# Kernel tuning notes

Hardware: AMD Instinct MI355X
Metric: run time of the kernel (lower is better)

Reference implementation:

```python
import jax, jax.numpy as jnp
import numpy as np

E = 8        # num experts
TOPK = 2
H = 1024     # hidden size
F = 4096     # ffn hidden size
SL, BS = 2048, 2
TOKENS = SL * BS
N = TOKENS * TOPK          # flattened routing assignments
CAP = (TOPK * TOKENS) // E # expert_capacity with capacity_factor=1.0


def setup_inputs() -> dict:
    key = jax.random.key(0)
    ks = jax.random.split(key, 6)
    x = jax.random.normal(ks[0], (SL, BS, H), jnp.float32)
    scores = jax.random.uniform(ks[1], (TOKENS, E), dtype=jnp.float32)
    expert_weights = jax.random.uniform(ks[2], (TOKENS, TOPK), dtype=jnp.float32)
    top_experts = jax.random.randint(ks[3], (TOKENS, TOPK), 0, E, dtype=jnp.int32)
    w1 = jax.random.normal(ks[4], (E, H, F), jnp.float32) * 0.02
    w2 = jax.random.normal(ks[5], (E, F, H), jnp.float32) * 0.02
    bias = jnp.zeros((H,), jnp.float32)
    return {"x": x, "scores": scores, "expert_weights": expert_weights,
            "top_experts": top_experts, "w1": w1, "w2": w2, "bias": bias}


def reference(x, scores, expert_weights, top_experts, w1, w2, bias):
    # --- indices_and_bins: stable sort tokens by expert, histogram, cumsum ---
    te = top_experts.reshape(-1)          # [N] int
    ew = expert_weights.reshape(-1)       # [N]
    xf = x.reshape(-1, H)                 # [TOKENS, H]

    indices = jnp.argsort(te)             # stable sort -> permutation [N]
    bin_ids = te[indices]                 # sorted expert ids [N]
    tpe = jax.ops.segment_sum(jnp.ones_like(te), te, num_segments=E)  # tokens per expert
    bins = jnp.cumsum(tpe)                # inclusive cumsum
    starts = bins - tpe                   # start offset of each expert's bin
    pos = jnp.arange(N) - starts[bin_ids] # position within expert bin [N]
    valid = pos < CAP                     # capacity drop mask
    tok = indices // TOPK                 # source token row for each assignment

    # --- binned_gather: [E, CAP, H], zero padded, tokens beyond capacity dropped ---
    dst = jnp.where(valid, pos, CAP)      # out-of-range -> dropped via mode='drop'
    buf = jnp.zeros((E, CAP, H), x.dtype).at[bin_ids, dst].set(xf[tok], mode='drop')

    # --- grouped MLP: per-expert gelu FFN ---
    h = jax.nn.gelu(jnp.einsum('ech,ehf->ecf', buf, w1), approximate=False)
    y = jnp.einsum('ecf,efh->ech', h, w2)

    # --- binned_scatter: weighted un-permute back to token order ---
    vals = y[bin_ids, jnp.where(valid, pos, 0)]                      # [N, H]
    w = jnp.where(valid, ew[indices], 0.0)[:, None]
    out = jnp.zeros((TOKENS, H), x.dtype).at[tok].add(vals * w)

    return out.reshape(x.shape) + bias
```

## Files before the change

### kernel.cpp

```cpp
#include <hip/hip_runtime.h>
#include <hip/hip_bf16.h>
#include <math.h>

#define NE 8
#define TOPK 2
#define HD 1024
#define FD 4096
#define NTOK 4096
#define NASSIGN 8192
#define CAP 1024

typedef __attribute__((ext_vector_type(8))) short short8;
typedef __attribute__((ext_vector_type(4))) float f32x4;
typedef __attribute__((ext_vector_type(4))) unsigned short us4;
typedef __attribute__((ext_vector_type(4))) unsigned int u32x4;

__device__ __forceinline__ unsigned short f2bf(float f) {
  unsigned u = __float_as_uint(f);
  u += 0x7fffu + ((u >> 16) & 1u);
  return (unsigned short)(u >> 16);
}

__device__ __forceinline__ void load_lds16(const void* g, void* l) {
  __builtin_amdgcn_global_load_lds((const __attribute__((address_space(1))) void*)g,
                                   (__attribute__((address_space(3))) void*)l, 16, 0, 0);
}

__device__ __forceinline__ unsigned swz(unsigned b) {
  return b ^ (((b >> 7) & 3u) << 4);
}

__global__ __launch_bounds__(256)
void transpose_convert(const float* __restrict__ W, unsigned short* __restrict__ Wt,
                       int R, int C) {
  __shared__ float tile[64][65];
  int e = blockIdx.z;
  W  += (size_t)e * R * C;
  Wt += (size_t)e * R * C;
  int c0 = blockIdx.x * 64, r0 = blockIdx.y * 64;
  int tx = threadIdx.x & 15, ty = threadIdx.x >> 4;
#pragma unroll
  for (int i = 0; i < 4; ++i) {
    f32x4 v = *(const f32x4*)(W + (size_t)(r0 + ty + i * 16) * C + c0 + tx * 4);
    tile[ty + i * 16][tx * 4 + 0] = v.x;
    tile[ty + i * 16][tx * 4 + 1] = v.y;
    tile[ty + i * 16][tx * 4 + 2] = v.z;
    tile[ty + i * 16][tx * 4 + 3] = v.w;
  }
  __syncthreads();
#pragma unroll
  for (int i = 0; i < 4; ++i) {
    int c = ty + i * 16;
    us4 o;
    o.x = f2bf(tile[tx * 4 + 0][c]);
    o.y = f2bf(tile[tx * 4 + 1][c]);
    o.z = f2bf(tile[tx * 4 + 2][c]);
    o.w = f2bf(tile[tx * 4 + 3][c]);
    *(us4*)(Wt + (size_t)(c0 + c) * R + r0 + tx * 4) = o;
  }
}

__global__ __launch_bounds__(1024)
void routing_kernel(const int* __restrict__ te, int* __restrict__ rankA,
                    int* __restrict__ srcTok, int* __restrict__ counts) {
  __shared__ uint4 pref[1024];
  int t = threadIdx.x;
  int myTe[8];
  unsigned lc[4] = {0, 0, 0, 0};
#pragma unroll
  for (int j = 0; j < 8; ++j) {
    int ee = te[t * 8 + j];
    myTe[j] = ee;
    lc[ee >> 1] += 1u << ((ee & 1) * 16);
  }
  uint4 inc;
  inc.x = lc[0]; inc.y = lc[1]; inc.z = lc[2]; inc.w = lc[3];
  pref[t] = inc;
  __syncthreads();
  for (int d = 1; d < 1024; d <<= 1) {
    uint4 add;
    bool has = (t >= d);
    if (has) add = pref[t - d];
    __syncthreads();
    if (has) {
      inc.x += add.x; inc.y += add.y; inc.z += add.z; inc.w += add.w;
      pref[t] = inc;
    }
    __syncthreads();
  }
  uint4 tot = pref[1023];
  unsigned ex[4] = {inc.x - lc[0], inc.y - lc[1], inc.z - lc[2], inc.w - lc[3]};
  int run[8];
#pragma unroll
  for (int eidx = 0; eidx < 8; ++eidx)
    run[eidx] = (ex[eidx >> 1] >> ((eidx & 1) * 16)) & 0xffff;
#pragma unroll
  for (int j = 0; j < 8; ++j) {
    int ee = myTe[j];
    int r = run[ee]++;
    rankA[t * 8 + j] = r;
    if (r < CAP) srcTok[ee * CAP + r] = (t * 8 + j) >> 1;
  }
  if (t < 8) {
    unsigned tt[4] = {tot.x, tot.y, tot.z, tot.w};
    counts[t] = (tt[t >> 1] >> ((t & 1) * 16)) & 0xffff;
  }
}

__global__ __launch_bounds__(128)
void gather_kernel(const float* __restrict__ x, const int* __restrict__ srcTok,
                   const int* __restrict__ counts, unsigned short* __restrict__ buf) {
  int row = blockIdx.x;
  int e = row >> 10;
  int c = row & (CAP - 1);
  int t = threadIdx.x;
  unsigned short* dst = buf + (size_t)row * HD + t * 8;
  if (c < counts[e]) {
    const float* src = x + (size_t)srcTok[row] * HD + t * 8;
    f32x4 v0 = *(const f32x4*)src;
    f32x4 v1 = *(const f32x4*)(src + 4);
    u32x4 o;
    o.x = f2bf(v0.x) | ((unsigned)f2bf(v0.y) << 16);
    o.y = f2bf(v0.z) | ((unsigned)f2bf(v0.w) << 16);
    o.z = f2bf(v1.x) | ((unsigned)f2bf(v1.y) << 16);
    o.w = f2bf(v1.z) | ((unsigned)f2bf(v1.w) << 16);
    *(u32x4*)dst = o;
  } else {
    u32x4 z = {0, 0, 0, 0};
    *(u32x4*)dst = z;
  }
}

template <int KTOT, int NDIM, int DO_GELU, int KSPLIT>
__global__ __launch_bounds__(512, 2)
void gemm256(const unsigned short* __restrict__ Ab, const unsigned short* __restrict__ Bb,
             void* __restrict__ Cv) {
  constexpr int KLOC = KTOT / KSPLIT;
  constexpr int NT = KLOC / 32;
  constexpr int GX = CAP / 256;
  constexpr int GY = NDIM / 256;
  constexpr int NWG = GX * GY * NE * KSPLIT;
  __shared__ char smem[4 * 32768];

  int orig = blockIdx.x;
  int wg = (orig & 7) * (NWG / 8) + (orig >> 3);
  int bx = wg % GX;
  int by = (wg / GX) % GY;
  int zz = wg / (GX * GY);
  int ks = zz % KSPLIT;
  int e  = zz / KSPLIT;

  const unsigned short* A  = Ab + (size_t)e * CAP * KTOT;
  const unsigned short* Bt = Bb + (size_t)e * NDIM * KTOT;
  int bm = bx * 256, bn = by * 256;
  int kbase = ks * KLOC;

  int tid = threadIdx.x;
  int lane = tid & 63;
  int w = tid >> 6;
  int wr = w >> 2, wc = w & 3;
  int l15 = lane & 15, lq = lane >> 4;

  unsigned offA[8], offB[4];
#pragma unroll
  for (int m = 0; m < 8; ++m)
    offA[m] = swz((unsigned)((wr * 128 + m * 16 + l15) * 64 + lq * 16));
#pragma unroll
  for (int n = 0; n < 4; ++n)
    offB[n] = swz((unsigned)((wc * 64 + n * 16 + l15) * 64 + lq * 16));

  const char* srcA[2]; const char* srcB[2];
  unsigned ldsOffA[2], ldsOffB[2];
#pragma unroll
  for (int i = 0; i < 2; ++i) {
    int idx = i * 512 + tid;
    int row = idx >> 2;
    unsigned kb = (unsigned)((idx & 3) * 16) ^ ((((unsigned)row >> 1) & 3u) << 4);
    srcA[i] = (const char*)A  + ((size_t)(bm + row) * KTOT + kbase) * 2 + kb;
    srcB[i] = (const char*)Bt + ((size_t)(bn + row) * KTOT + kbase) * 2 + kb;
    ldsOffA[i] = (unsigned)idx * 16;
    ldsOffB[i] = 16384u + (unsigned)idx * 16;
  }

#pragma unroll
  for (int tt = 0; tt < 3; ++tt) {
    char* db = smem + tt * 32768;
#pragma unroll
    for (int i = 0; i < 2; ++i) {
      load_lds16(srcA[i] + tt * 64, db + ldsOffA[i]);
      load_lds16(srcB[i] + tt * 64, db + ldsOffB[i]);
    }
  }
  srcA[0] += 192; srcA[1] += 192; srcB[0] += 192; srcB[1] += 192;
  asm volatile("s_waitcnt vmcnt(8)\ns_barrier" ::: "memory");

  f32x4 acc[8][4] = {};

  auto step = [&](int t, int bufi) {
    if (t + 3 < NT) {
      char* db = smem + ((bufi + 3) & 3) * 32768;
#pragma unroll
      for (int i = 0; i < 2; ++i) {
        load_lds16(srcA[i], db + ldsOffA[i]);
        load_lds16(srcB[i], db + ldsOffB[i]);
      }
      srcA[0] += 64; srcA[1] += 64; srcB[0] += 64; srcB[1] += 64;
    }
    const char* rb = smem + bufi * 32768;
    short8 af[8], bf[4];
#pragma unroll
    for (int m = 0; m < 8; ++m) af[m] = *(const short8*)(rb + offA[m]);
#pragma unroll
    for (int n = 0; n < 4; ++n) bf[n] = *(const short8*)(rb + 16384 + offB[n]);
    asm volatile("s_waitcnt lgkmcnt(0)" ::: "memory");
    __builtin_amdgcn_sched_barrier(0);
    __builtin_amdgcn_s_setprio(1);
#pragma unroll
    for (int m = 0; m < 8; ++m)
#pragma unroll
      for (int n = 0; n < 4; ++n)
        acc[m][n] = __builtin_amdgcn_mfma_f32_16x16x32_bf16(af[m], bf[n], acc[m][n], 0, 0, 0);
    __builtin_amdgcn_s_setprio(0);
    __builtin_amdgcn_sched_barrier(0);
    asm volatile("s_waitcnt vmcnt(8)\ns_barrier" ::: "memory");
  };

  for (int t = 0; t < NT; t += 4) {
    step(t + 0, 0);
    step(t + 1, 1);
    step(t + 2, 2);
    step(t + 3, 3);
  }

  int r0 = bm + wr * 128 + lq * 4;
  int c0 = bn + wc * 64 + l15;
  if (DO_GELU) {
    unsigned short* C = (unsigned short*)Cv + (size_t)e * CAP * NDIM;
#pragma unroll
    for (int m = 0; m < 8; ++m)
#pragma unroll
      for (int n = 0; n < 4; ++n)
#pragma unroll
        for (int j = 0; j < 4; ++j) {
          float v = acc[m][n][j];
          float y = 0.7978845608028654f * (v + 0.044715f * v * v * v);
          float g = v / (1.0f + __expf(-2.0f * y));
          C[(size_t)(r0 + m * 16 + j) * NDIM + (c0 + n * 16)] = f2bf(g);
        }
  } else {
    float* C = (float*)Cv + ((size_t)ks * NE + e) * CAP * NDIM;
#pragma unroll
    for (int m = 0; m < 8; ++m)
#pragma unroll
      for (int n = 0; n < 4; ++n)
#pragma unroll
        for (int j = 0; j < 4; ++j)
          C[(size_t)(r0 + m * 16 + j) * NDIM + (c0 + n * 16)] = acc[m][n][j];
  }
}

__global__ __launch_bounds__(128)
void scatter_kernel(const float* __restrict__ y, const int* __restrict__ te,
                    const int* __restrict__ rankA, const float* __restrict__ ew,
                    const float* __restrict__ bias, float* __restrict__ out) {
  int tk = blockIdx.x;
  int t = threadIdx.x;
  f32x4 a0 = *(const f32x4*)(bias + t * 8);
  f32x4 a1 = *(const f32x4*)(bias + t * 8 + 4);
#pragma unroll
  for (int k = 0; k < TOPK; ++k) {
    int a = tk * TOPK + k;
    int r = rankA[a];
    if (r < CAP) {
      float wgt = ew[a];
      size_t rowoff = ((size_t)te[a] * CAP + r) * HD + t * 8;
      const float* y0 = y + rowoff;
      const float* y1 = y + (size_t)NE * CAP * HD + rowoff;
      f32x4 v0 = *(const f32x4*)y0 + *(const f32x4*)y1;
      f32x4 v1 = *(const f32x4*)(y0 + 4) + *(const f32x4*)(y1 + 4);
      a0 += wgt * v0;
      a1 += wgt * v1;
    }
  }
  float* o = out + (size_t)tk * HD + t * 8;
  *(f32x4*)o = a0;
  *(f32x4*)(o + 4) = a1;
}

extern "C" void kernel_launch(void* const* d_in, const int* in_sizes, int n_in,
                              void* d_out, int out_size, void* d_ws, size_t ws_size,
                              hipStream_t stream) {
  const float* x    = (const float*)d_in[0];
  const float* ew   = (const float*)d_in[2];
  const int*   te   = (const int*)d_in[3];
  const float* w1   = (const float*)d_in[4];
  const float* w2   = (const float*)d_in[5];
  const float* bias = (const float*)d_in[6];
  float* out = (float*)d_out;

  unsigned short* w1t  = (unsigned short*)d_ws;
  unsigned short* w2t  = w1t + (size_t)NE * HD * FD;
  unsigned short* bufg = w2t + (size_t)NE * HD * FD;
  unsigned short* hbuf = bufg + (size_t)NE * CAP * HD;
  float*          ybuf = (float*)w1t;
  int* rankA  = (int*)(hbuf + (size_t)NE * CAP * FD);
  int* srcTok = rankA + NASSIGN;
  int* counts = srcTok + NE * CAP;

  transpose_convert<<<dim3(FD / 64, HD / 64, NE), 256, 0, stream>>>(w1, w1t, HD, FD);
  transpose_convert<<<dim3(HD / 64, FD / 64, NE), 256, 0, stream>>>(w2, w2t, FD, HD);
  routing_kernel<<<1, 1024, 0, stream>>>(te, rankA, srcTok, counts);
  gather_kernel<<<NE * CAP, 128, 0, stream>>>(x, srcTok, counts, bufg);
  gemm256<HD, FD, 1, 1><<<512, 512, 0, stream>>>(bufg, w1t, (void*)hbuf);
  gemm256<FD, HD, 0, 2><<<256, 512, 0, stream>>>(hbuf, w2t, (void*)ybuf);
  scatter_kernel<<<NTOK, 128, 0, stream>>>(ybuf, te, rankA, ew, bias, out);
}
```

Before: 278.4 us.

## Restructure expert GEMM mainloop into double-buffered 64-wide K tiles with quadrant-interleaved loads

The GEMM mainloop moves from a 4-stage ring of 32-wide K tiles to two 64KB buffers holding 64-wide K tiles. Each tile's output is computed in four quadrants, and each quadrant's MFMA burst is interleaved with issuing a slice of the next tiles' global-to-LDS loads, separated by barriers. It also switches to an XOR swizzle over 128-byte rows to avoid LDS bank conflicts. The aim is to hide load latency behind compute and cut per-tile overhead, at the cost of more barriers per iteration and redundant wrap-around loads on the last iterations.

```diff
diff --git a/kernel.cpp b/kernel.cpp
--- a/kernel.cpp
+++ b/kernel.cpp
@@ -24,10 +24,6 @@
 __device__ __forceinline__ void load_lds16(const void* g, void* l) {
   __builtin_amdgcn_global_load_lds((const __attribute__((address_space(1))) void*)g,
                                    (__attribute__((address_space(3))) void*)l, 16, 0, 0);
-}
-
-__device__ __forceinline__ unsigned swz(unsigned b) {
-  return b ^ (((b >> 7) & 3u) << 4);
 }
 
 __global__ __launch_bounds__(256)
@@ -136,11 +132,11 @@
 void gemm256(const unsigned short* __restrict__ Ab, const unsigned short* __restrict__ Bb,
              void* __restrict__ Cv) {
   constexpr int KLOC = KTOT / KSPLIT;
-  constexpr int NT = KLOC / 32;
+  constexpr int NT = KLOC / 64;
   constexpr int GX = CAP / 256;
   constexpr int GY = NDIM / 256;
   constexpr int NWG = GX * GY * NE * KSPLIT;
-  __shared__ char smem[4 * 32768];
+  __shared__ char smem[131072];
 
   int orig = blockIdx.x;
   int wg = (orig & 7) * (NWG / 8) + (orig >> 3);
@@ -161,76 +157,135 @@
   int wr = w >> 2, wc = w & 3;
   int l15 = lane & 15, lq = lane >> 4;
 
-  unsigned offA[8], offB[4];
-#pragma unroll
-  for (int m = 0; m < 8; ++m)
-    offA[m] = swz((unsigned)((wr * 128 + m * 16 + l15) * 64 + lq * 16));
-#pragma unroll
-  for (int n = 0; n < 4; ++n)
-    offB[n] = swz((unsigned)((wc * 64 + n * 16 + l15) * 64 + lq * 16));
-
-  const char* srcA[2]; const char* srcB[2];
-  unsigned ldsOffA[2], ldsOffB[2];
-#pragma unroll
-  for (int i = 0; i < 2; ++i) {
-    int idx = i * 512 + tid;
-    int row = idx >> 2;
-    unsigned kb = (unsigned)((idx & 3) * 16) ^ ((((unsigned)row >> 1) & 3u) << 4);
-    srcA[i] = (const char*)A  + ((size_t)(bm + row) * KTOT + kbase) * 2 + kb;
-    srcB[i] = (const char*)Bt + ((size_t)(bn + row) * KTOT + kbase) * 2 + kb;
-    ldsOffA[i] = (unsigned)idx * 16;
-    ldsOffB[i] = 16384u + (unsigned)idx * 16;
-  }
-
-#pragma unroll
-  for (int tt = 0; tt < 3; ++tt) {
-    char* db = smem + tt * 32768;
-#pragma unroll
-    for (int i = 0; i < 2; ++i) {
-      load_lds16(srcA[i] + tt * 64, db + ldsOffA[i]);
-      load_lds16(srcB[i] + tt * 64, db + ldsOffB[i]);
-    }
-  }
-  srcA[0] += 192; srcA[1] += 192; srcB[0] += 192; srcB[1] += 192;
-  asm volatile("s_waitcnt vmcnt(8)\ns_barrier" ::: "memory");
+  unsigned sw0 = (unsigned)((lq ^ (l15 & 7)) * 16);
+  unsigned sw1 = (unsigned)(((4 + lq) ^ (l15 & 7)) * 16);
+  unsigned aBase = (unsigned)((wr * 64 + l15) * 128);
+  unsigned bBase = 32768u + (unsigned)((wc * 32 + l15) * 128);
+
+  const char* sA[2][2];
+  const char* sB[2][2];
+  unsigned dAo[2][2], dBo[2][2];
+#pragma unroll
+  for (int h = 0; h < 2; ++h)
+#pragma unroll
+    for (int j = 0; j < 2; ++j) {
+      int blk = j * 512 + tid;
+      int rl = blk >> 3, s = blk & 7;
+      int g = s ^ (rl & 7);
+      int rowA = ((rl >> 6) << 7) + h * 64 + (rl & 63);
+      int rowB = ((rl >> 5) << 6) + h * 32 + (rl & 31);
+      sA[h][j] = (const char*)(A  + (size_t)(bm + rowA) * KTOT + kbase + g * 8);
+      sB[h][j] = (const char*)(Bt + (size_t)(bn + rowB) * KTOT + kbase + g * 8);
+      dAo[h][j] = (unsigned)(h * 16384 + blk * 16);
+      dBo[h][j] = (unsigned)(32768 + h * 16384 + blk * 16);
+    }
+
+#define STAGE_A(h, dbase, kt) { \
+    load_lds16(sA[h][0] + (size_t)(kt) * 128, smem + (dbase) + dAo[h][0]); \
+    load_lds16(sA[h][1] + (size_t)(kt) * 128, smem + (dbase) + dAo[h][1]); }
+#define STAGE_B(h, dbase, kt) { \
+    load_lds16(sB[h][0] + (size_t)(kt) * 128, smem + (dbase) + dBo[h][0]); \
+    load_lds16(sB[h][1] + (size_t)(kt) * 128, smem + (dbase) + dBo[h][1]); }
+
+  STAGE_A(0, 0, 0); STAGE_B(0, 0, 0); STAGE_B(1, 0, 0); STAGE_A(1, 0, 0);
+  STAGE_A(0, 65536, 1); STAGE_B(0, 65536, 1); STAGE_B(1, 65536, 1);
+  asm volatile("s_waitcnt vmcnt(6)" ::: "memory");
+  __builtin_amdgcn_s_barrier();
 
   f32x4 acc[8][4] = {};
-
-  auto step = [&](int t, int bufi) {
-    if (t + 3 < NT) {
-      char* db = smem + ((bufi + 3) & 3) * 32768;
-#pragma unroll
-      for (int i = 0; i < 2; ++i) {
-        load_lds16(srcA[i], db + ldsOffA[i]);
-        load_lds16(srcB[i], db + ldsOffB[i]);
-      }
-      srcA[0] += 64; srcA[1] += 64; srcB[0] += 64; srcB[1] += 64;
-    }
-    const char* rb = smem + bufi * 32768;
-    short8 af[8], bf[4];
-#pragma unroll
-    for (int m = 0; m < 8; ++m) af[m] = *(const short8*)(rb + offA[m]);
-#pragma unroll
-    for (int n = 0; n < 4; ++n) bf[n] = *(const short8*)(rb + 16384 + offB[n]);
+  short8 af[4][2], bl[2][2], bh[2][2];
+
+  for (int t = 0; t < NT; ++t) {
+    unsigned cb = (t & 1) ? 65536u : 0u;
+    unsigned nb = cb ^ 65536u;
+    int kt1 = (t + 1 < NT) ? t + 1 : 0;
+    int kt2 = (t + 2 < NT) ? t + 2 : 0;
+
+#pragma unroll
+    for (int m = 0; m < 4; ++m) {
+      af[m][0] = *(const short8*)(smem + cb + aBase + m * 2048 + sw0);
+      af[m][1] = *(const short8*)(smem + cb + aBase + m * 2048 + sw1);
+    }
+#pragma unroll
+    for (int n = 0; n < 2; ++n) {
+      bl[n][0] = *(const short8*)(smem + cb + bBase + n * 2048 + sw0);
+      bl[n][1] = *(const short8*)(smem + cb + bBase + n * 2048 + sw1);
+    }
+    STAGE_A(1, nb, kt1);
+    __builtin_amdgcn_s_barrier();
     asm volatile("s_waitcnt lgkmcnt(0)" ::: "memory");
     __builtin_amdgcn_sched_barrier(0);
     __builtin_amdgcn_s_setprio(1);
 #pragma unroll
-    for (int m = 0; m < 8; ++m)
-#pragma unroll
-      for (int n = 0; n < 4; ++n)
-        acc[m][n] = __builtin_amdgcn_mfma_f32_16x16x32_bf16(af[m], bf[n], acc[m][n], 0, 0, 0);
+    for (int k2 = 0; k2 < 2; ++k2)
+#pragma unroll
+      for (int m = 0; m < 4; ++m)
+#pragma unroll
+        for (int n = 0; n < 2; ++n)
+          acc[m][n] = __builtin_amdgcn_mfma_f32_16x16x32_bf16(af[m][k2], bl[n][k2], acc[m][n], 0, 0, 0);
     __builtin_amdgcn_s_setprio(0);
     __builtin_amdgcn_sched_barrier(0);
-    asm volatile("s_waitcnt vmcnt(8)\ns_barrier" ::: "memory");
-  };
-
-  for (int t = 0; t < NT; t += 4) {
-    step(t + 0, 0);
-    step(t + 1, 1);
-    step(t + 2, 2);
-    step(t + 3, 3);
-  }
+    __builtin_amdgcn_s_barrier();
+
+#pragma unroll
+    for (int n = 0; n < 2; ++n) {
+      bh[n][0] = *(const short8*)(smem + cb + bBase + 16384 + n * 2048 + sw0);
+      bh[n][1] = *(const short8*)(smem + cb + bBase + 16384 + n * 2048 + sw1);
+    }
+    STAGE_A(0, cb, kt2);
+    __builtin_amdgcn_s_barrier();
+    asm volatile("s_waitcnt lgkmcnt(0)" ::: "memory");
+    __builtin_amdgcn_sched_barrier(0);
+    __builtin_amdgcn_s_setprio(1);
+#pragma unroll
+    for (int k2 = 0; k2 < 2; ++k2)
+#pragma unroll
+      for (int m = 0; m < 4; ++m)
+#pragma unroll
+        for (int n = 0; n < 2; ++n)
+          acc[m][n + 2] = __builtin_amdgcn_mfma_f32_16x16x32_bf16(af[m][k2], bh[n][k2], acc[m][n + 2], 0, 0, 0);
+    __builtin_amdgcn_s_setprio(0);
+    __builtin_amdgcn_sched_barrier(0);
+    __builtin_amdgcn_s_barrier();
+
+#pragma unroll
+    for (int m = 0; m < 4; ++m) {
+      af[m][0] = *(const short8*)(smem + cb + aBase + 16384 + m * 2048 + sw0);
+      af[m][1] = *(const short8*)(smem + cb + aBase + 16384 + m * 2048 + sw1);
+    }
+    STAGE_B(0, cb, kt2);
+    __builtin_amdgcn_s_barrier();
+    asm volatile("s_waitcnt lgkmcnt(0)" ::: "memory");
+    __builtin_amdgcn_sched_barrier(0);
+    __builtin_amdgcn_s_setprio(1);
+#pragma unroll
+    for (int k2 = 0; k2 < 2; ++k2)
+#pragma unroll
+      for (int m = 0; m < 4; ++m)
+#pragma unroll
+        for (int n = 0; n < 2; ++n)
+          acc[m + 4][n + 2] = __builtin_amdgcn_mfma_f32_16x16x32_bf16(af[m][k2], bh[n][k2], acc[m + 4][n + 2], 0, 0, 0);
+    __builtin_amdgcn_s_setprio(0);
+    __builtin_amdgcn_sched_barrier(0);
+    __builtin_amdgcn_s_barrier();
+
+    STAGE_B(1, cb, kt2);
+    __builtin_amdgcn_s_barrier();
+    __builtin_amdgcn_s_setprio(1);
+#pragma unroll
+    for (int k2 = 0; k2 < 2; ++k2)
+#pragma unroll
+      for (int m = 0; m < 4; ++m)
+#pragma unroll
+        for (int n = 0; n < 2; ++n)
+          acc[m + 4][n] = __builtin_amdgcn_mfma_f32_16x16x32_bf16(af[m][k2], bl[n][k2], acc[m + 4][n], 0, 0, 0);
+    __builtin_amdgcn_s_setprio(0);
+    __builtin_amdgcn_sched_barrier(0);
+    asm volatile("s_waitcnt vmcnt(6)" ::: "memory");
+    __builtin_amdgcn_s_barrier();
+  }
+#undef STAGE_A
+#undef STAGE_B
 
   int r0 = bm + wr * 128 + lq * 4;
   int c0 = bn + wc * 64 + l15;
```

New measurement: 250.5 us. -10.0%, faster.

## Interleave LDS fragment prefetch and split global loads with MFMA halves

Applied to the files above, without the earlier changes.

Restructures the GEMM main loop so the next tile's A/B fragments are prefetched from LDS into double-buffered registers while the current tile's MFMAs run. Each tile's MFMAs are split into two halves, with the A and B global-to-LDS loads issued separately between them. The vmcnt wait is relaxed from 8 to 4 to match the new load grouping. The aim is to hide LDS read latency and spread memory issue across compute, at the cost of more live registers and tighter correctness reasoning about buffer reuse with a 4-stage ring.

```diff
diff --git a/kernel.cpp b/kernel.cpp
--- a/kernel.cpp
+++ b/kernel.cpp
@@ -161,76 +161,99 @@
   int wr = w >> 2, wc = w & 3;
   int l15 = lane & 15, lq = lane >> 4;
 
-  unsigned offA[8], offB[4];
+  unsigned aoff[8], boff[4];
 #pragma unroll
   for (int m = 0; m < 8; ++m)
-    offA[m] = swz((unsigned)((wr * 128 + m * 16 + l15) * 64 + lq * 16));
+    aoff[m] = swz((unsigned)((wr * 128 + m * 16 + l15) * 64 + lq * 16));
 #pragma unroll
   for (int n = 0; n < 4; ++n)
-    offB[n] = swz((unsigned)((wc * 64 + n * 16 + l15) * 64 + lq * 16));
-
-  const char* srcA[2]; const char* srcB[2];
-  unsigned ldsOffA[2], ldsOffB[2];
-#pragma unroll
-  for (int i = 0; i < 2; ++i) {
-    int idx = i * 512 + tid;
-    int row = idx >> 2;
-    unsigned kb = (unsigned)((idx & 3) * 16) ^ ((((unsigned)row >> 1) & 3u) << 4);
-    srcA[i] = (const char*)A  + ((size_t)(bm + row) * KTOT + kbase) * 2 + kb;
-    srcB[i] = (const char*)Bt + ((size_t)(bn + row) * KTOT + kbase) * 2 + kb;
-    ldsOffA[i] = (unsigned)idx * 16;
-    ldsOffB[i] = 16384u + (unsigned)idx * 16;
+    boff[n] = swz((unsigned)((wc * 64 + n * 16 + l15) * 64 + lq * 16));
+
+  const char *srcA0, *srcA1, *srcB0, *srcB1;
+  unsigned dA0, dA1, dB0, dB1;
+  {
+    int idx0 = tid, idx1 = 512 + tid;
+    int r0_ = idx0 >> 2, r1_ = idx1 >> 2;
+    unsigned kb0 = ((unsigned)(idx0 & 3) * 16) ^ ((((unsigned)r0_ >> 1) & 3u) << 4);
+    unsigned kb1 = ((unsigned)(idx1 & 3) * 16) ^ ((((unsigned)r1_ >> 1) & 3u) << 4);
+    srcA0 = (const char*)(A  + (size_t)(bm + r0_) * KTOT + kbase) + kb0;
+    srcA1 = (const char*)(A  + (size_t)(bm + r1_) * KTOT + kbase) + kb1;
+    srcB0 = (const char*)(Bt + (size_t)(bn + r0_) * KTOT + kbase) + kb0;
+    srcB1 = (const char*)(Bt + (size_t)(bn + r1_) * KTOT + kbase) + kb1;
+    dA0 = (unsigned)idx0 * 16; dA1 = (unsigned)idx1 * 16;
+    dB0 = 16384u + (unsigned)idx0 * 16; dB1 = 16384u + (unsigned)idx1 * 16;
   }
 
 #pragma unroll
   for (int tt = 0; tt < 3; ++tt) {
     char* db = smem + tt * 32768;
-#pragma unroll
-    for (int i = 0; i < 2; ++i) {
-      load_lds16(srcA[i] + tt * 64, db + ldsOffA[i]);
-      load_lds16(srcB[i] + tt * 64, db + ldsOffB[i]);
-    }
-  }
-  srcA[0] += 192; srcA[1] += 192; srcB[0] += 192; srcB[1] += 192;
-  asm volatile("s_waitcnt vmcnt(8)\ns_barrier" ::: "memory");
+    load_lds16(srcA0 + tt * 64, db + dA0);
+    load_lds16(srcA1 + tt * 64, db + dA1);
+    load_lds16(srcB0 + tt * 64, db + dB0);
+    load_lds16(srcB1 + tt * 64, db + dB1);
+  }
+  srcA0 += 192; srcA1 += 192; srcB0 += 192; srcB1 += 192;
+  asm volatile("s_waitcnt vmcnt(4)" ::: "memory");
+  __builtin_amdgcn_s_barrier();
 
   f32x4 acc[8][4] = {};
-
-  auto step = [&](int t, int bufi) {
-    if (t + 3 < NT) {
-      char* db = smem + ((bufi + 3) & 3) * 32768;
-#pragma unroll
-      for (int i = 0; i < 2; ++i) {
-        load_lds16(srcA[i], db + ldsOffA[i]);
-        load_lds16(srcB[i], db + ldsOffB[i]);
-      }
-      srcA[0] += 64; srcA[1] += 64; srcB[0] += 64; srcB[1] += 64;
-    }
-    const char* rb = smem + bufi * 32768;
-    short8 af[8], bf[4];
-#pragma unroll
-    for (int m = 0; m < 8; ++m) af[m] = *(const short8*)(rb + offA[m]);
-#pragma unroll
-    for (int n = 0; n < 4; ++n) bf[n] = *(const short8*)(rb + 16384 + offB[n]);
-    asm volatile("s_waitcnt lgkmcnt(0)" ::: "memory");
-    __builtin_amdgcn_sched_barrier(0);
-    __builtin_amdgcn_s_setprio(1);
-#pragma unroll
-    for (int m = 0; m < 8; ++m)
-#pragma unroll
-      for (int n = 0; n < 4; ++n)
-        acc[m][n] = __builtin_amdgcn_mfma_f32_16x16x32_bf16(af[m], bf[n], acc[m][n], 0, 0, 0);
-    __builtin_amdgcn_s_setprio(0);
-    __builtin_amdgcn_sched_barrier(0);
-    asm volatile("s_waitcnt vmcnt(8)\ns_barrier" ::: "memory");
-  };
-
-  for (int t = 0; t < NT; t += 4) {
-    step(t + 0, 0);
-    step(t + 1, 1);
-    step(t + 2, 2);
-    step(t + 3, 3);
-  }
+  short8 afLo0[4], afLo1[4], bf0[4], bf1[4], af47[4];
+
+#pragma unroll
+  for (int j = 0; j < 4; ++j) afLo0[j] = *(const short8*)(smem + aoff[j]);
+#pragma unroll
+  for (int n = 0; n < 4; ++n) bf0[n]  = *(const short8*)(smem + 16384 + boff[n]);
+
+#define TILE(T, CUR, NXT)                                                         \
+  {                                                                               \
+    const int t_ = (T);                                                           \
+    const char* rb_ = smem + (t_ & 3) * 32768;                                    \
+    _Pragma("unroll") for (int j = 0; j < 4; ++j)                                 \
+        af47[j] = *(const short8*)(rb_ + aoff[4 + j]);                            \
+    if (t_ + 3 < NT) {                                                            \
+      char* db_ = smem + ((t_ + 3) & 3) * 32768;                                  \
+      load_lds16(srcA0, db_ + dA0);                                               \
+      load_lds16(srcA1, db_ + dA1);                                               \
+    }                                                                             \
+    __builtin_amdgcn_sched_barrier(0);                                            \
+    __builtin_amdgcn_s_setprio(1);                                                \
+    _Pragma("unroll") for (int m = 0; m < 4; ++m)                                 \
+      _Pragma("unroll") for (int n = 0; n < 4; ++n)                               \
+        acc[m][n] = __builtin_amdgcn_mfma_f32_16x16x32_bf16(                      \
+            afLo##CUR[m], bf##CUR[n], acc[m][n], 0, 0, 0);                        \
+    __builtin_amdgcn_s_setprio(0);                                                \
+    __builtin_amdgcn_sched_barrier(0);                                            \
+    if (t_ + 1 < NT) {                                                            \
+      const char* rn_ = smem + ((t_ + 1) & 3) * 32768;                            \
+      _Pragma("unroll") for (int j = 0; j < 4; ++j)                               \
+          afLo##NXT[j] = *(const short8*)(rn_ + aoff[j]);                         \
+      _Pragma("unroll") for (int n = 0; n < 4; ++n)                               \
+          bf##NXT[n] = *(const short8*)(rn_ + 16384 + boff[n]);                   \
+    }                                                                             \
+    if (t_ + 3 < NT) {                                                            \
+      char* db_ = smem + ((t_ + 3) & 3) * 32768;                                  \
+      load_lds16(srcB0, db_ + dB0);                                               \
+      load_lds16(srcB1, db_ + dB1);                                               \
+    }                                                                             \
+    __builtin_amdgcn_sched_barrier(0);                                            \
+    __builtin_amdgcn_s_setprio(1);                                                \
+    _Pragma("unroll") for (int m = 0; m < 4; ++m)                                 \
+      _Pragma("unroll") for (int n = 0; n < 4; ++n)                               \
+        acc[m + 4][n] = __builtin_amdgcn_mfma_f32_16x16x32_bf16(                  \
+            af47[m], bf##CUR[n], acc[m + 4][n], 0, 0, 0);                         \
+    __builtin_amdgcn_s_setprio(0);                                                \
+    __builtin_amdgcn_sched_barrier(0);                                            \
+    asm volatile("s_waitcnt vmcnt(4)" ::: "memory");                              \
+    __builtin_amdgcn_s_barrier();                                                 \
+    srcA0 += 64; srcA1 += 64; srcB0 += 64; srcB1 += 64;                           \
+  }
+
+#pragma unroll 1
+  for (int t = 0; t < NT; t += 2) {
+    TILE(t, 0, 1);
+    TILE(t + 1, 1, 0);
+  }
+#undef TILE
 
   int r0 = bm + wr * 128 + lq * 4;
   int c0 = bn + wc * 64 + l15;
```

After: 258.0 us. 7.3% less time.

## Fuse weight fp32-to-bf16 transpose conversion into GEMM B-tile loading

Applied to the files above, without the earlier changes.

Drops the two standalone transpose_convert kernels and has each GEMM workgroup read fp32 weights directly, convert them to bf16 in registers and write them swizzled into LDS, using a register-staged pipeline alongside the async A loads. This removes a full read and write pass over both weight tensors and two kernel launches. In exchange each weight tile is re-read and re-converted by every M-block workgroup (4 per expert), the fp32 global traffic for B doubles per tile, and conversion ALU work now sits in the GEMM main loop, which is no longer unrolled.

```diff
diff --git a/kernel.cpp b/kernel.cpp
--- a/kernel.cpp
+++ b/kernel.cpp
@@ -12,7 +12,7 @@
 
 typedef __attribute__((ext_vector_type(8))) short short8;
 typedef __attribute__((ext_vector_type(4))) float f32x4;
-typedef __attribute__((ext_vector_type(4))) unsigned short us4;
+typedef __attribute__((ext_vector_type(2))) unsigned int u32x2;
 typedef __attribute__((ext_vector_type(4))) unsigned int u32x4;
 
 __device__ __forceinline__ unsigned short f2bf(float f) {
@@ -28,36 +28,6 @@
 
 __device__ __forceinline__ unsigned swz(unsigned b) {
   return b ^ (((b >> 7) & 3u) << 4);
-}
-
-__global__ __launch_bounds__(256)
-void transpose_convert(const float* __restrict__ W, unsigned short* __restrict__ Wt,
-                       int R, int C) {
-  __shared__ float tile[64][65];
-  int e = blockIdx.z;
-  W  += (size_t)e * R * C;
-  Wt += (size_t)e * R * C;
-  int c0 = blockIdx.x * 64, r0 = blockIdx.y * 64;
-  int tx = threadIdx.x & 15, ty = threadIdx.x >> 4;
-#pragma unroll
-  for (int i = 0; i < 4; ++i) {
-    f32x4 v = *(const f32x4*)(W + (size_t)(r0 + ty + i * 16) * C + c0 + tx * 4);
-    tile[ty + i * 16][tx * 4 + 0] = v.x;
-    tile[ty + i * 16][tx * 4 + 1] = v.y;
-    tile[ty + i * 16][tx * 4 + 2] = v.z;
-    tile[ty + i * 16][tx * 4 + 3] = v.w;
-  }
-  __syncthreads();
-#pragma unroll
-  for (int i = 0; i < 4; ++i) {
-    int c = ty + i * 16;
-    us4 o;
-    o.x = f2bf(tile[tx * 4 + 0][c]);
-    o.y = f2bf(tile[tx * 4 + 1][c]);
-    o.z = f2bf(tile[tx * 4 + 2][c]);
-    o.w = f2bf(tile[tx * 4 + 3][c]);
-    *(us4*)(Wt + (size_t)(c0 + c) * R + r0 + tx * 4) = o;
-  }
 }
 
 __global__ __launch_bounds__(1024)
@@ -133,8 +103,8 @@
 
 template <int KTOT, int NDIM, int DO_GELU, int KSPLIT>
 __global__ __launch_bounds__(512, 2)
-void gemm256(const unsigned short* __restrict__ Ab, const unsigned short* __restrict__ Bb,
-             void* __restrict__ Cv) {
+void gemm256f(const unsigned short* __restrict__ Ab, const float* __restrict__ Bf,
+              void* __restrict__ Cv) {
   constexpr int KLOC = KTOT / KSPLIT;
   constexpr int NT = KLOC / 32;
   constexpr int GX = CAP / 256;
@@ -150,8 +120,8 @@
   int ks = zz % KSPLIT;
   int e  = zz / KSPLIT;
 
-  const unsigned short* A  = Ab + (size_t)e * CAP * KTOT;
-  const unsigned short* Bt = Bb + (size_t)e * NDIM * KTOT;
+  const unsigned short* A = Ab + (size_t)e * CAP * KTOT;
+  const float* B = Bf + (size_t)e * KTOT * NDIM;
   int bm = bx * 256, bn = by * 256;
   int kbase = ks * KLOC;
 
@@ -161,57 +131,92 @@
   int wr = w >> 2, wc = w & 3;
   int l15 = lane & 15, lq = lane >> 4;
 
-  unsigned offA[8], offB[4];
+  unsigned aoff[8], boff[4];
 #pragma unroll
   for (int m = 0; m < 8; ++m)
-    offA[m] = swz((unsigned)((wr * 128 + m * 16 + l15) * 64 + lq * 16));
+    aoff[m] = swz((unsigned)((wr * 128 + m * 16 + l15) * 64 + lq * 16));
 #pragma unroll
   for (int n = 0; n < 4; ++n)
-    offB[n] = swz((unsigned)((wc * 64 + n * 16 + l15) * 64 + lq * 16));
-
-  const char* srcA[2]; const char* srcB[2];
-  unsigned ldsOffA[2], ldsOffB[2];
-#pragma unroll
-  for (int i = 0; i < 2; ++i) {
-    int idx = i * 512 + tid;
-    int row = idx >> 2;
-    unsigned kb = (unsigned)((idx & 3) * 16) ^ ((((unsigned)row >> 1) & 3u) << 4);
-    srcA[i] = (const char*)A  + ((size_t)(bm + row) * KTOT + kbase) * 2 + kb;
-    srcB[i] = (const char*)Bt + ((size_t)(bn + row) * KTOT + kbase) * 2 + kb;
-    ldsOffA[i] = (unsigned)idx * 16;
-    ldsOffB[i] = 16384u + (unsigned)idx * 16;
-  }
+    boff[n] = 16384u + swz((unsigned)((wc * 64 + n * 16 + l15) * 64 + lq * 16));
+
+  const char *srcA0, *srcA1;
+  unsigned dA0, dA1;
+  {
+    int i0 = tid, i1 = 512 + tid;
+    int r0_ = i0 >> 2, r1_ = i1 >> 2;
+    unsigned kb0 = ((unsigned)(i0 & 3) * 16) ^ ((((unsigned)r0_ >> 1) & 3u) << 4);
+    unsigned kb1 = ((unsigned)(i1 & 3) * 16) ^ ((((unsigned)r1_ >> 1) & 3u) << 4);
+    srcA0 = (const char*)(A + (size_t)(bm + r0_) * KTOT + kbase) + kb0;
+    srcA1 = (const char*)(A + (size_t)(bm + r1_) * KTOT + kbase) + kb1;
+    dA0 = (unsigned)i0 * 16;
+    dA1 = (unsigned)i1 * 16;
+  }
+
+  const float* srcB;
+  unsigned wB[4];
+  {
+    int bk = (lane & 7) * 4;
+    int bnq = w * 32 + (lane >> 3) * 4;
+    srcB = B + (size_t)(kbase + bk) * NDIM + (bn + bnq);
+    unsigned g = (unsigned)((lane & 7) >> 1);
+    unsigned h = (unsigned)(lane & 1);
+#pragma unroll
+    for (int i = 0; i < 4; ++i) {
+      unsigned row = (unsigned)(w * 32 + (lane >> 3) * 4 + i);
+      wB[i] = 16384u + row * 64 + ((g ^ ((row >> 1) & 3u)) << 4) + h * 8;
+    }
+  }
+
+  f32x4 br[4];
+
+#define LOADB() { \
+    br[0] = *(const f32x4*)(srcB);            \
+    br[1] = *(const f32x4*)(srcB + NDIM);     \
+    br[2] = *(const f32x4*)(srcB + 2 * NDIM); \
+    br[3] = *(const f32x4*)(srcB + 3 * NDIM); \
+    srcB += 32 * (size_t)NDIM; }
+
+#define CVTB(bi) { \
+    char* db_ = smem + (bi) * 32768; \
+    _Pragma("unroll") for (int i_ = 0; i_ < 4; ++i_) { \
+      unsigned lo_ = f2bf(br[0][i_]) | ((unsigned)f2bf(br[1][i_]) << 16); \
+      unsigned hi_ = f2bf(br[2][i_]) | ((unsigned)f2bf(br[3][i_]) << 16); \
+      u32x2 v_; v_.x = lo_; v_.y = hi_; \
+      *(u32x2*)(db_ + wB[i_]) = v_; } }
 
 #pragma unroll
   for (int tt = 0; tt < 3; ++tt) {
     char* db = smem + tt * 32768;
-#pragma unroll
-    for (int i = 0; i < 2; ++i) {
-      load_lds16(srcA[i] + tt * 64, db + ldsOffA[i]);
-      load_lds16(srcB[i] + tt * 64, db + ldsOffB[i]);
+    load_lds16(srcA0 + tt * 64, db + dA0);
+    load_lds16(srcA1 + tt * 64, db + dA1);
+  }
+  srcA0 += 192; srcA1 += 192;
+  LOADB();
+  asm volatile("s_waitcnt vmcnt(0)" ::: "memory");
+  CVTB(0);
+  LOADB();
+  asm volatile("s_waitcnt vmcnt(0)" ::: "memory");
+  CVTB(1);
+  LOADB();
+  asm volatile("s_waitcnt lgkmcnt(0)" ::: "memory");
+  asm volatile("s_barrier" ::: "memory");
+
+  f32x4 acc[8][4] = {};
+
+#pragma unroll 1
+  for (int t = 0; t < NT; ++t) {
+    const char* rb = smem + (t & 3) * 32768;
+    short8 af[8], bfv[4];
+#pragma unroll
+    for (int m = 0; m < 8; ++m) af[m] = *(const short8*)(rb + aoff[m]);
+#pragma unroll
+    for (int n = 0; n < 4; ++n) bfv[n] = *(const short8*)(rb + boff[n]);
+    if (t + 3 < NT) {
+      char* db = smem + ((t + 3) & 3) * 32768;
+      load_lds16(srcA0, db + dA0);
+      load_lds16(srcA1, db + dA1);
+      srcA0 += 64; srcA1 += 64;
     }
-  }
-  srcA[0] += 192; srcA[1] += 192; srcB[0] += 192; srcB[1] += 192;
-  asm volatile("s_waitcnt vmcnt(8)\ns_barrier" ::: "memory");
-
-  f32x4 acc[8][4] = {};
-
-  auto step = [&](int t, int bufi) {
-    if (t + 3 < NT) {
-      char* db = smem + ((bufi + 3) & 3) * 32768;
-#pragma unroll
-      for (int i = 0; i < 2; ++i) {
-        load_lds16(srcA[i], db + ldsOffA[i]);
-        load_lds16(srcB[i], db + ldsOffB[i]);
-      }
-      srcA[0] += 64; srcA[1] += 64; srcB[0] += 64; srcB[1] += 64;
-    }
-    const char* rb = smem + bufi * 32768;
-    short8 af[8], bf[4];
-#pragma unroll
-    for (int m = 0; m < 8; ++m) af[m] = *(const short8*)(rb + offA[m]);
-#pragma unroll
-    for (int n = 0; n < 4; ++n) bf[n] = *(const short8*)(rb + 16384 + offB[n]);
     asm volatile("s_waitcnt lgkmcnt(0)" ::: "memory");
     __builtin_amdgcn_sched_barrier(0);
     __builtin_amdgcn_s_setprio(1);
@@ -219,18 +224,17 @@
     for (int m = 0; m < 8; ++m)
 #pragma unroll
       for (int n = 0; n < 4; ++n)
-        acc[m][n] = __builtin_amdgcn_mfma_f32_16x16x32_bf16(af[m], bf[n], acc[m][n], 0, 0, 0);
+        acc[m][n] = __builtin_amdgcn_mfma_f32_16x16x32_bf16(af[m], bfv[n], acc[m][n], 0, 0, 0);
     __builtin_amdgcn_s_setprio(0);
-    __builtin_amdgcn_sched_barrier(0);
-    asm volatile("s_waitcnt vmcnt(8)\ns_barrier" ::: "memory");
-  };
-
-  for (int t = 0; t < NT; t += 4) {
-    step(t + 0, 0);
-    step(t + 1, 1);
-    step(t + 2, 2);
-    step(t + 3, 3);
-  }
+    if (t + 3 < NT) asm volatile("s_waitcnt vmcnt(2)" ::: "memory");
+    else            asm volatile("s_waitcnt vmcnt(0)" ::: "memory");
+    if (t + 2 < NT) CVTB((t + 2) & 3);
+    if (t + 3 < NT) LOADB();
+    asm volatile("s_waitcnt lgkmcnt(0)" ::: "memory");
+    asm volatile("s_barrier" ::: "memory");
+  }
+#undef LOADB
+#undef CVTB
 
   int r0 = bm + wr * 128 + lq * 4;
   int c0 = bn + wc * 64 + l15;
@@ -298,20 +302,16 @@
   const float* bias = (const float*)d_in[6];
   float* out = (float*)d_out;
 
-  unsigned short* w1t  = (unsigned short*)d_ws;
-  unsigned short* w2t  = w1t + (size_t)NE * HD * FD;
-  unsigned short* bufg = w2t + (size_t)NE * HD * FD;
+  unsigned short* bufg = (unsigned short*)d_ws;
   unsigned short* hbuf = bufg + (size_t)NE * CAP * HD;
-  float*          ybuf = (float*)w1t;
-  int* rankA  = (int*)(hbuf + (size_t)NE * CAP * FD);
+  float*          ybuf = (float*)(hbuf + (size_t)NE * CAP * FD);
+  int* rankA  = (int*)(ybuf + (size_t)2 * NE * CAP * HD);
   int* srcTok = rankA + NASSIGN;
   int* counts = srcTok + NE * CAP;
 
-  transpose_convert<<<dim3(FD / 64, HD / 64, NE), 256, 0, stream>>>(w1, w1t, HD, FD);
-  transpose_convert<<<dim3(HD / 64, FD / 64, NE), 256, 0, stream>>>(w2, w2t, FD, HD);
   routing_kernel<<<1, 1024, 0, stream>>>(te, rankA, srcTok, counts);
   gather_kernel<<<NE * CAP, 128, 0, stream>>>(x, srcTok, counts, bufg);
-  gemm256<HD, FD, 1, 1><<<512, 512, 0, stream>>>(bufg, w1t, (void*)hbuf);
-  gemm256<FD, HD, 0, 2><<<256, 512, 0, stream>>>(hbuf, w2t, (void*)ybuf);
+  gemm256f<HD, FD, 1, 1><<<512, 512, 0, stream>>>(bufg, w1, (void*)hbuf);
+  gemm256f<FD, HD, 0, 2><<<256, 512, 0, stream>>>(hbuf, w2, (void*)ybuf);
   scatter_kernel<<<NTOK, 128, 0, stream>>>(ybuf, te, rankA, ew, bias, out);
 }
```

After: 279.4 us. No clear change (+0.4%).
